# Performance work log

Hardware: AMD Instinct MI355X
Metric: run time of the kernel (lower is better)

Reference implementation:

```python
import jax, jax.numpy as jnp
import numpy as np
from jax import lax

ROUNDS = 64
HIDDEN = 256
BATCH = 16384


def setup_inputs() -> dict:
    key = jax.random.key(0)
    k1, k2, k3 = jax.random.split(key, 3)
    # state: (B, 256) bits in {0,1} as float32 (output of bytes_to_bits)
    state = jax.random.bernoulli(k1, 0.5, (BATCH, HIDDEN)).astype(jnp.float32)
    # matrices: (64, 256, 256) ternary values in {-1,0,1} (byte % 3 - 1)
    matrices = jax.random.randint(k2, (ROUNDS, HIDDEN, HIDDEN), -1, 2).astype(jnp.float32)
    # noise: (B, 64, 256) bits in {0,1} derived from sha256 of the nonce
    noise = jax.random.bernoulli(k3, 0.5, (BATCH, ROUNDS, HIDDEN)).astype(jnp.float32)
    return {"state": state, "matrices": matrices, "noise": noise}


def reference(state, matrices, noise):
    # 64-round recurrence: s <- (floor(s @ M_r^T + n_r)) mod 2
    noise_r = jnp.transpose(noise, (1, 0, 2))  # (R, B, H)

    def step(s, xs):
        M, n = xs  # M: (H,H), n: (B,H)
        s = jnp.remainder(jnp.floor(s @ M.T + n), 2.0)
        return s, None

    final, _ = lax.scan(step, state, (matrices, noise_r))
    return final  # (B, 256) bits as float32
```

## Files before the change

kernel.cpp:

```cpp
#include <hip/hip_runtime.h>

typedef unsigned int u32;
typedef unsigned long long u64;

#define R_ROUNDS 64
#define HID 256
#define BATCH 16384
#define RPW 4


__global__ __launch_bounds__(256) void pack_matrices_kernel(
        const float* __restrict__ M, u32* __restrict__ P) {
    const int lane = threadIdx.x & 63;
    const int gw   = (int)((blockIdx.x * blockDim.x + threadIdx.x) >> 6);
    const int r    = gw >> 8;
    const int jj   = gw & 255;
    const float4 v = *(const float4*)(M + (size_t)gw * HID + 4 * lane);
    const u64 b0 = __ballot(v.x != 0.0f);
    const u64 b1 = __ballot(v.y != 0.0f);
    const u64 b2 = __ballot(v.z != 0.0f);
    const u64 b3 = __ballot(v.w != 0.0f);
    if (lane < 8) {
        const int w = lane;
        u64 bb = b0;
        if ((w >> 1) == 1) bb = b1;
        if ((w >> 1) == 2) bb = b2;
        if ((w >> 1) == 3) bb = b3;
        const u32 val = (w & 1) ? (u32)(bb >> 32) : (u32)bb;
        const int t = 2 * (jj & 3) + (w >> 2);
        P[r * 2048 + t * 256 + (jj >> 2) * 4 + (w & 3)] = val;
    }
}

__global__ __launch_bounds__(256, 4) void tenshash_kernel(
        const float* __restrict__ state,
        const u32*  __restrict__ pA,
        const float* __restrict__ noise,
        float* __restrict__ out) {
    const int lane = threadIdx.x & 63;
    const int warp = threadIdx.x >> 6;
    const int wave = (int)(blockIdx.x * 4 + warp);
    const int row0 = wave * RPW;

    __shared__ u32 smem[2][2048];

    u64 S0[RPW], S1[RPW], S2[RPW], S3[RPW];
#pragma unroll
    for (int rw = 0; rw < RPW; ++rw) {
        const float4 v = *(const float4*)(state + (size_t)(row0 + rw) * HID + 4 * lane);
        S0[rw] = __ballot(v.x != 0.0f);
        S1[rw] = __ballot(v.y != 0.0f);
        S2[rw] = __ballot(v.z != 0.0f);
        S3[rw] = __ballot(v.w != 0.0f);
    }

    const float* no_l = noise + (size_t)row0 * (R_ROUNDS * HID) + 4 * lane;

    auto STAGE = [&](int r, int b) {
        const char* g = (const char*)(pA + (size_t)r * 2048);
#pragma unroll
        for (int t = 2 * warp; t < 2 * warp + 2; ++t) {
            __builtin_amdgcn_global_load_lds(
                (const __attribute__((address_space(1))) void*)
                    (g + t * 1024 + lane * 16),
                (__attribute__((address_space(3))) void*)&smem[b][t * 256],
                16, 0, 0);
        }
    };
    auto LOADN = [&](float4* n, int r) {
#pragma unroll
        for (int rw = 0; rw < RPW; ++rw)
            n[rw] = *(const float4*)(no_l + (size_t)rw * (R_ROUNDS * HID) + r * HID);
    };
    auto RUN = [&](const u32* base, const float4* n) {
        const uint4* p = (const uint4*)base;
        uint4 a[8];
#pragma unroll
        for (int t = 0; t < 8; ++t)
            a[t] = p[(t << 6) + lane];
#pragma unroll
        for (int rw = 0; rw < RPW; ++rw) {
            u64 ns0, ns1, ns2, ns3;
#pragma unroll
            for (int i = 0; i < 4; ++i) {
                const u64 W0 = (u64)a[2 * i].x     | ((u64)a[2 * i].y     << 32);
                const u64 W1 = (u64)a[2 * i].z     | ((u64)a[2 * i].w     << 32);
                const u64 W2 = (u64)a[2 * i + 1].x | ((u64)a[2 * i + 1].y << 32);
                const u64 W3 = (u64)a[2 * i + 1].z | ((u64)a[2 * i + 1].w << 32);
                const float nfv = (i == 0) ? n[rw].x : (i == 1) ? n[rw].y
                                : (i == 2) ? n[rw].z : n[rw].w;
                const u32 c = (u32)__popcll(W0 & S0[rw]) + (u32)__popcll(W1 & S1[rw])
                            + (u32)__popcll(W2 & S2[rw]) + (u32)__popcll(W3 & S3[rw])
                            + (u32)nfv;
                const u64 nb = __ballot((c & 1u) != 0);
                if (i == 0) ns0 = nb; else if (i == 1) ns1 = nb;
                else if (i == 2) ns2 = nb; else ns3 = nb;
            }
            S0[rw] = ns0; S1[rw] = ns1; S2[rw] = ns2; S3[rw] = ns3;
        }
    };

    float4 nA[RPW], nB[RPW];

    LOADN(nA, 0);
    STAGE(0, 0);
    __syncthreads();
#pragma unroll 1
    for (int r = 0; r < R_ROUNDS; r += 2) {
        LOADN(nB, r + 1);
        STAGE(r + 1, 1);
        RUN(&smem[0][0], nA);
        __syncthreads();
        if (r + 2 < R_ROUNDS) {
            LOADN(nA, r + 2);
            STAGE(r + 2, 0);
        }
        RUN(&smem[1][0], nB);
        __syncthreads();
    }

#pragma unroll
    for (int rw = 0; rw < RPW; ++rw) {
        float4 o;
        o.x = (float)((u32)(S0[rw] >> lane) & 1u);
        o.y = (float)((u32)(S1[rw] >> lane) & 1u);
        o.z = (float)((u32)(S2[rw] >> lane) & 1u);
        o.w = (float)((u32)(S3[rw] >> lane) & 1u);
        *(float4*)(out + (size_t)(row0 + rw) * HID + 4 * lane) = o;
    }
}

extern "C" void kernel_launch(void* const* d_in, const int* in_sizes, int n_in,
                              void* d_out, int out_size, void* d_ws, size_t ws_size,
                              hipStream_t stream) {
    const float* state = (const float*)d_in[0];
    const float* mats  = (const float*)d_in[1];
    const float* noise = (const float*)d_in[2];
    float* out         = (float*)d_out;
    u32* pA            = (u32*)d_ws;

    pack_matrices_kernel<<<(R_ROUNDS * HID) / 4, 256, 0, stream>>>(mats, pA);

    const int blocks = (BATCH / RPW) / 4;
    tenshash_kernel<<<blocks, 256, 0, stream>>>(state, pA, noise, out);
}
```

Before: 234.4 us.

## Deepen matrix/noise prefetch to four LDS buffers with partial vmcnt waits

Replaces the double-buffered staging with a four-slot ring. Each phase prefetches matrix and noise data two rounds ahead, then uses a raw barrier with s_waitcnt vmcnt(6) instead of __syncthreads, so newer loads stay in flight. RUN is also reordered to loop over rows inside each word group, loading the matrix words from LDS per group instead of all eight uint4 up front. In exchange it doubles LDS use per block, which may reduce occupancy, and it relies on hand-counted vmcnt values that are fragile if the compiler changes load counts.

```diff
diff --git a/kernel.cpp b/kernel.cpp
--- a/kernel.cpp
+++ b/kernel.cpp
@@ -42,7 +42,7 @@
     const int wave = (int)(blockIdx.x * 4 + warp);
     const int row0 = wave * RPW;
 
-    __shared__ u32 smem[2][2048];
+    __shared__ u32 smem[4][2048];
 
     u64 S0[RPW], S1[RPW], S2[RPW], S3[RPW];
 #pragma unroll
@@ -74,50 +74,61 @@
     };
     auto RUN = [&](const u32* base, const float4* n) {
         const uint4* p = (const uint4*)base;
-        uint4 a[8];
+        u64 ns0[RPW], ns1[RPW], ns2[RPW], ns3[RPW];
 #pragma unroll
-        for (int t = 0; t < 8; ++t)
-            a[t] = p[(t << 6) + lane];
+        for (int i = 0; i < 4; ++i) {
+            const uint4 a0 = p[((2 * i) << 6) + lane];
+            const uint4 a1 = p[((2 * i + 1) << 6) + lane];
+            const u64 W0 = (u64)a0.x | ((u64)a0.y << 32);
+            const u64 W1 = (u64)a0.z | ((u64)a0.w << 32);
+            const u64 W2 = (u64)a1.x | ((u64)a1.y << 32);
+            const u64 W3 = (u64)a1.z | ((u64)a1.w << 32);
 #pragma unroll
-        for (int rw = 0; rw < RPW; ++rw) {
-            u64 ns0, ns1, ns2, ns3;
-#pragma unroll
-            for (int i = 0; i < 4; ++i) {
-                const u64 W0 = (u64)a[2 * i].x     | ((u64)a[2 * i].y     << 32);
-                const u64 W1 = (u64)a[2 * i].z     | ((u64)a[2 * i].w     << 32);
-                const u64 W2 = (u64)a[2 * i + 1].x | ((u64)a[2 * i + 1].y << 32);
-                const u64 W3 = (u64)a[2 * i + 1].z | ((u64)a[2 * i + 1].w << 32);
+            for (int rw = 0; rw < RPW; ++rw) {
                 const float nfv = (i == 0) ? n[rw].x : (i == 1) ? n[rw].y
                                 : (i == 2) ? n[rw].z : n[rw].w;
                 const u32 c = (u32)__popcll(W0 & S0[rw]) + (u32)__popcll(W1 & S1[rw])
                             + (u32)__popcll(W2 & S2[rw]) + (u32)__popcll(W3 & S3[rw])
                             + (u32)nfv;
                 const u64 nb = __ballot((c & 1u) != 0);
-                if (i == 0) ns0 = nb; else if (i == 1) ns1 = nb;
-                else if (i == 2) ns2 = nb; else ns3 = nb;
+                if (i == 0) ns0[rw] = nb; else if (i == 1) ns1[rw] = nb;
+                else if (i == 2) ns2[rw] = nb; else ns3[rw] = nb;
             }
-            S0[rw] = ns0; S1[rw] = ns1; S2[rw] = ns2; S3[rw] = ns3;
+        }
+#pragma unroll
+        for (int rw = 0; rw < RPW; ++rw) {
+            S0[rw] = ns0[rw]; S1[rw] = ns1[rw];
+            S2[rw] = ns2[rw]; S3[rw] = ns3[rw];
         }
     };
 
-    float4 nA[RPW], nB[RPW];
+    float4 n0[RPW], n1[RPW], n2[RPW], n3[RPW];
 
-    LOADN(nA, 0);
-    STAGE(0, 0);
-    __syncthreads();
+    STAGE(0, 0); LOADN(n0, 0);
+    STAGE(1, 1); LOADN(n1, 1);
+    asm volatile("s_waitcnt vmcnt(6)" ::: "memory");
+    __builtin_amdgcn_s_barrier();
+    __builtin_amdgcn_sched_barrier(0);
+
+#define PHASE(k, NUSE, NLOAD)                                            \
+    {                                                                    \
+        int rs = r + k + 2; if (rs > R_ROUNDS - 1) rs = R_ROUNDS - 1;    \
+        STAGE(rs, (k + 2) & 3);                                          \
+        LOADN(NLOAD, rs);                                                \
+        RUN(&smem[k][0], NUSE);                                          \
+        asm volatile("s_waitcnt vmcnt(6)" ::: "memory");                 \
+        __builtin_amdgcn_s_barrier();                                    \
+        __builtin_amdgcn_sched_barrier(0);                               \
+    }
+
 #pragma unroll 1
-    for (int r = 0; r < R_ROUNDS; r += 2) {
-        LOADN(nB, r + 1);
-        STAGE(r + 1, 1);
-        RUN(&smem[0][0], nA);
-        __syncthreads();
-        if (r + 2 < R_ROUNDS) {
-            LOADN(nA, r + 2);
-            STAGE(r + 2, 0);
-        }
-        RUN(&smem[1][0], nB);
-        __syncthreads();
+    for (int r = 0; r < R_ROUNDS; r += 4) {
+        PHASE(0, n0, n2)
+        PHASE(1, n1, n3)
+        PHASE(2, n2, n0)
+        PHASE(3, n3, n1)
     }
+#undef PHASE
 
 #pragma unroll
     for (int rw = 0; rw < RPW; ++rw) {
```

Result: faster. 227.7 us, median of 2 (-2.9%).
